# Kernel optimization log

Hardware: AMD Instinct MI355X
Metric: run time of the kernel (lower is better)

## Reference

```python
import jax, jax.numpy as jnp
import numpy as np

N_NODES = 50000
N_COLORS = 256
D = 64
H = 128  # MLP hidden = 2*D
E_VV = 800000
E_VC = 400000


def _mlp_params(key, d_in, d_hid, d_out):
    k1, k2 = jax.random.split(key)
    s1 = 1.0 / np.sqrt(d_in)
    s2 = 1.0 / np.sqrt(d_hid)
    return (
        jax.random.uniform(k1, (d_in, d_hid), jnp.float32, -s1, s1),
        jnp.zeros((d_hid,), jnp.float32),
        jax.random.uniform(k2, (d_hid, d_out), jnp.float32, -s2, s2),
        jnp.zeros((d_out,), jnp.float32),
    )


def setup_inputs() -> dict:
    key = jax.random.key(0)
    ks = jax.random.split(key, 8)
    x_v = jax.random.normal(ks[0], (N_NODES, D), jnp.float32)
    x_c = jax.random.normal(ks[1], (N_COLORS, D), jnp.float32)
    src_vv = jax.random.randint(ks[2], (E_VV,), 0, N_NODES, jnp.int32)
    dst_vv = jax.random.randint(ks[3], (E_VV,), 0, N_NODES, jnp.int32)
    src_vc = jax.random.randint(ks[4], (E_VC,), 0, N_COLORS, jnp.int32)
    dst_vc = jax.random.randint(ks[5], (E_VC,), 0, N_NODES, jnp.int32)
    W1v, b1v, W2v, b2v = _mlp_params(ks[6], D, H, D)
    W1c, b1c, W2c, b2c = _mlp_params(ks[7], D, H, D)
    return {
        "x_v": x_v, "x_c": x_c,
        "W1v": W1v, "b1v": b1v, "W2v": W2v, "b2v": b2v,
        "W1c": W1c, "b1c": b1c, "W2c": W2c, "b2c": b2c,
        "src_vv": src_vv, "dst_vv": dst_vv,
        "src_vc": src_vc, "dst_vc": dst_vc,
    }


def reference(x_v, x_c, W1v, b1v, W2v, b2v, W1c, b1c, W2c, b2c,
              src_vv, dst_vv, src_vc, dst_vc):
    n = x_v.shape[0]
    # vertex->vertex messages: gather, MLP, scatter-sum
    mv = jax.nn.relu(x_v[src_vv] @ W1v + b1v) @ W2v + b2v  # [E_vv, D]
    agg_v = jax.ops.segment_sum(mv, dst_vv, num_segments=n)
    # color->vertex messages: gather color embeddings, MLP, scatter-sum
    mc = jax.nn.relu(x_c[src_vc] @ W1c + b1c) @ W2c + b2c  # [E_vc, D]
    agg_c = jax.ops.segment_sum(mc, dst_vc, num_segments=n)
    return jax.nn.relu(x_v + agg_v + agg_c)
```

## Files before the change

### kernel.cpp

```cpp
#include <hip/hip_runtime.h>

#define NN 50000
#define NC 256
#define DD 64
#define HH 128
#define EVV 800000
#define EVC 400000
#define NE 1200000
#define NB 196
#define BCAP 8192
#define MLPV_B 3125
#define MLPC_B 16
#define MLP_B (MLPV_B + MLPC_B)
#define FILL_EPB 2048
#define FILL_B 586
#define K1_B (FILL_B * 7)
#define GAT_B (NB * 8)
#define VCAP 64

__device__ __forceinline__ unsigned short f2bf(float x) {
  unsigned u = __float_as_uint(x);
  u = (u + 0x7fffu + ((u >> 16) & 1u)) >> 16;
  return (unsigned short)u;
}

union SMem {
  struct {
    float xs[4][64][4];
    float hs[4][128][4];
  } m;
  struct {
    int cnt[NB];
    int off[NB];
    int gbase[NB];
    int sa[256], sb[256];
    unsigned int stage[FILL_EPB];
  } f;
};

__device__ __forceinline__ void mlp16(
    const float* __restrict__ X, const float* __restrict__ W1,
    const float* __restrict__ b1, const float* __restrict__ W2,
    const float* __restrict__ b2, unsigned short* __restrict__ Y, int blk,
    int nrows, float (*xs)[64][4], float (*hs)[128][4]) {
  const int wave = threadIdx.x >> 6;
  const int lane = threadIdx.x & 63;
  const int row0 = (blk * 4 + wave) * 4;

  {
    float4 a;
    a.x = (row0 + 0 < nrows) ? X[(row0 + 0) * DD + lane] : 0.f;
    a.y = (row0 + 1 < nrows) ? X[(row0 + 1) * DD + lane] : 0.f;
    a.z = (row0 + 2 < nrows) ? X[(row0 + 2) * DD + lane] : 0.f;
    a.w = (row0 + 3 < nrows) ? X[(row0 + 3) * DD + lane] : 0.f;
    *(float4*)&xs[wave][lane][0] = a;
  }

  const float bias0 = b1[lane];
  const float bias1 = b1[lane + 64];
  float h0[4], h1[4];
#pragma unroll
  for (int r = 0; r < 4; ++r) { h0[r] = bias0; h1[r] = bias1; }

#pragma unroll 8
  for (int k = 0; k < 64; ++k) {
    const float4 xa = *(const float4*)&xs[wave][k][0];
    const float wa = W1[k * HH + lane];
    const float wb = W1[k * HH + 64 + lane];
    h0[0] = fmaf(xa.x, wa, h0[0]); h1[0] = fmaf(xa.x, wb, h1[0]);
    h0[1] = fmaf(xa.y, wa, h0[1]); h1[1] = fmaf(xa.y, wb, h1[1]);
    h0[2] = fmaf(xa.z, wa, h0[2]); h1[2] = fmaf(xa.z, wb, h1[2]);
    h0[3] = fmaf(xa.w, wa, h0[3]); h1[3] = fmaf(xa.w, wb, h1[3]);
  }
  *(float4*)&hs[wave][lane][0] =
      make_float4(fmaxf(h0[0], 0.f), fmaxf(h0[1], 0.f), fmaxf(h0[2], 0.f),
                  fmaxf(h0[3], 0.f));
  *(float4*)&hs[wave][lane + 64][0] =
      make_float4(fmaxf(h1[0], 0.f), fmaxf(h1[1], 0.f), fmaxf(h1[2], 0.f),
                  fmaxf(h1[3], 0.f));

  const float bias2 = b2[lane];
  float a[4];
#pragma unroll
  for (int r = 0; r < 4; ++r) a[r] = bias2;

#pragma unroll 8
  for (int j = 0; j < HH; ++j) {
    const float4 ha = *(const float4*)&hs[wave][j][0];
    const float w = W2[j * DD + lane];
    a[0] = fmaf(ha.x, w, a[0]);
    a[1] = fmaf(ha.y, w, a[1]);
    a[2] = fmaf(ha.z, w, a[2]);
    a[3] = fmaf(ha.w, w, a[3]);
  }
#pragma unroll
  for (int r = 0; r < 4; ++r)
    if (row0 + r < nrows) Y[(row0 + r) * DD + lane] = f2bf(a[r]);
}

__device__ __forceinline__ void fill_block(
    const int* __restrict__ src_vv, const int* __restrict__ dst_vv,
    const int* __restrict__ src_vc, const int* __restrict__ dst_vc,
    int* __restrict__ gcur, unsigned int* __restrict__ records, int blk,
    SMem* sm) {
  const int t = threadIdx.x;
  const int base = blk * FILL_EPB;
  if (t < NB) sm->f.cnt[t] = 0;
  __syncthreads();

  unsigned int rec[8];
  int rk[8];
#pragma unroll
  for (int r = 0; r < 8; ++r) {
    const int e = base + r * 256 + t;
    rk[r] = -1;
    if (e < NE) {
      int s, d;
      if (e < EVV) {
        s = src_vv[e];
        d = dst_vv[e];
      } else {
        s = NN + src_vc[e - EVV];
        d = dst_vc[e - EVV];
      }
      rec[r] = ((unsigned int)d << 16) | (unsigned int)s;
      rk[r] = atomicAdd(&sm->f.cnt[d >> 8], 1);
    }
  }
  __syncthreads();

  const int val = (t < NB) ? sm->f.cnt[t] : 0;
  sm->f.sa[t] = val;
  __syncthreads();
  int* s = sm->f.sa;
  int* d = sm->f.sb;
  for (int o = 1; o < 256; o <<= 1) {
    d[t] = s[t] + ((t >= o) ? s[t - o] : 0);
    __syncthreads();
    int* tmp = s; s = d; d = tmp;
  }
  if (t < NB) {
    sm->f.off[t] = s[t] - val;
    sm->f.gbase[t] = t * BCAP + ((val > 0) ? atomicAdd(&gcur[t], val) : 0);
  }
  __syncthreads();

#pragma unroll
  for (int r = 0; r < 8; ++r)
    if (rk[r] >= 0) sm->f.stage[sm->f.off[rec[r] >> 24] + rk[r]] = rec[r];
  __syncthreads();

  const int total = (NE - base < FILL_EPB) ? (NE - base) : FILL_EPB;
  for (int i = t; i < total; i += 256) {
    const unsigned int u = sm->f.stage[i];
    const int b2 = u >> 24;
    records[sm->f.gbase[b2] + (i - sm->f.off[b2])] = u;
  }
}

__global__ __launch_bounds__(256) void k1_kernel(
    const float* __restrict__ x_v, const float* __restrict__ x_c,
    const float* __restrict__ W1v, const float* __restrict__ b1v,
    const float* __restrict__ W2v, const float* __restrict__ b2v,
    const float* __restrict__ W1c, const float* __restrict__ b1c,
    const float* __restrict__ W2c, const float* __restrict__ b2c,
    const int* __restrict__ src_vv, const int* __restrict__ dst_vv,
    const int* __restrict__ src_vc, const int* __restrict__ dst_vc,
    unsigned short* __restrict__ table, int* __restrict__ gcur,
    unsigned int* __restrict__ records) {
  __shared__ SMem sm;
  const int q = blockIdx.x / 7;
  const int r = blockIdx.x % 7;
  if (r == 0) {
    fill_block(src_vv, dst_vv, src_vc, dst_vc, gcur, records, q, &sm);
  } else {
    const int mb = q * 6 + (r - 1);
    if (mb >= MLP_B) return;
    if (mb < MLPV_B)
      mlp16(x_v, W1v, b1v, W2v, b2v, table, mb, NN, sm.m.xs, sm.m.hs);
    else
      mlp16(x_c, W1c, b1c, W2c, b2c, table + (size_t)NN * DD, mb - MLPV_B, NC,
            sm.m.xs, sm.m.hs);
  }
}

__device__ __forceinline__ void acc8(float* a, const uint4 t) {
  a[0] += __uint_as_float(t.x << 16);
  a[1] += __uint_as_float(t.x & 0xffff0000u);
  a[2] += __uint_as_float(t.y << 16);
  a[3] += __uint_as_float(t.y & 0xffff0000u);
  a[4] += __uint_as_float(t.z << 16);
  a[5] += __uint_as_float(t.z & 0xffff0000u);
  a[6] += __uint_as_float(t.w << 16);
  a[7] += __uint_as_float(t.w & 0xffff0000u);
}

__device__ __forceinline__ void place(unsigned int u, int sub, int* c1,
                                      unsigned short* slots) {
  const int dd = u >> 16;
  if (((dd >> 5) & 7) == sub) {
    const int lv = dd & 31;
    const int pos = atomicAdd(&c1[lv], 1);
    if (pos < VCAP) slots[lv * VCAP + pos] = (unsigned short)(u & 0xffffu);
  }
}

__global__ __launch_bounds__(256) void gather_kernel(
    const uint4* __restrict__ table4, const unsigned int* __restrict__ records,
    const int* __restrict__ gcur, const float4* __restrict__ xv4,
    float4* __restrict__ out4) {
  __shared__ int c1[32];
  __shared__ unsigned short slots[32 * VCAP];
  const int t = threadIdx.x;
  const int bucket = blockIdx.x >> 3;
  const int sub = blockIdx.x & 7;
  const int start = bucket * BCAP;
  const int nrec = gcur[bucket];

  const int g = t >> 3;
  const int c = t & 7;
  const int v = bucket * 256 + sub * 32 + g;
  const size_t ob = (size_t)v * 16 + c * 2;
  float4 x0 = {0.f, 0.f, 0.f, 0.f}, x1 = x0;
  if (v < NN) {
    x0 = xv4[ob];
    x1 = xv4[ob + 1];
  }

  if (t < 32) c1[t] = 0;
  __syncthreads();

  const uint4* rec4 = (const uint4*)(records + start);
  const int nfull = nrec >> 2;
  for (int q = t; q < nfull; q += 256) {
    const uint4 u = rec4[q];
    place(u.x, sub, c1, slots);
    place(u.y, sub, c1, slots);
    place(u.z, sub, c1, slots);
    place(u.w, sub, c1, slots);
  }
  for (int j = (nfull << 2) + t; j < nrec; j += 256)
    place(records[start + j], sub, c1, slots);
  __syncthreads();

  if (v >= NN) return;
  int n = c1[g];
  n = (n > VCAP) ? VCAP : n;
  const unsigned short* sl = slots + g * VCAP;

  float a[8];
#pragma unroll
  for (int r = 0; r < 8; ++r) a[r] = 0.f;

  int i = 0;
  for (; i + 8 <= n; i += 8) {
    const int e0 = sl[i + 0];
    const int e1 = sl[i + 1];
    const int e2 = sl[i + 2];
    const int e3 = sl[i + 3];
    const int e4 = sl[i + 4];
    const int e5 = sl[i + 5];
    const int e6 = sl[i + 6];
    const int e7 = sl[i + 7];
    const uint4 t0 = table4[(size_t)e0 * 8 + c];
    const uint4 t1 = table4[(size_t)e1 * 8 + c];
    const uint4 t2 = table4[(size_t)e2 * 8 + c];
    const uint4 t3 = table4[(size_t)e3 * 8 + c];
    const uint4 t4 = table4[(size_t)e4 * 8 + c];
    const uint4 t5 = table4[(size_t)e5 * 8 + c];
    const uint4 t6 = table4[(size_t)e6 * 8 + c];
    const uint4 t7 = table4[(size_t)e7 * 8 + c];
    acc8(a, t0); acc8(a, t1); acc8(a, t2); acc8(a, t3);
    acc8(a, t4); acc8(a, t5); acc8(a, t6); acc8(a, t7);
  }
  for (; i + 4 <= n; i += 4) {
    const int e0 = sl[i + 0];
    const int e1 = sl[i + 1];
    const int e2 = sl[i + 2];
    const int e3 = sl[i + 3];
    const uint4 t0 = table4[(size_t)e0 * 8 + c];
    const uint4 t1 = table4[(size_t)e1 * 8 + c];
    const uint4 t2 = table4[(size_t)e2 * 8 + c];
    const uint4 t3 = table4[(size_t)e3 * 8 + c];
    acc8(a, t0); acc8(a, t1); acc8(a, t2); acc8(a, t3);
  }
  for (; i < n; ++i) {
    const uint4 t0 = table4[(size_t)sl[i] * 8 + c];
    acc8(a, t0);
  }

  float4 o0, o1;
  o0.x = fmaxf(x0.x + a[0], 0.f);
  o0.y = fmaxf(x0.y + a[1], 0.f);
  o0.z = fmaxf(x0.z + a[2], 0.f);
  o0.w = fmaxf(x0.w + a[3], 0.f);
  o1.x = fmaxf(x1.x + a[4], 0.f);
  o1.y = fmaxf(x1.y + a[5], 0.f);
  o1.z = fmaxf(x1.z + a[6], 0.f);
  o1.w = fmaxf(x1.w + a[7], 0.f);
  out4[ob] = o0;
  out4[ob + 1] = o1;
}

extern "C" void kernel_launch(void* const* d_in, const int* in_sizes, int n_in,
                              void* d_out, int out_size, void* d_ws,
                              size_t ws_size, hipStream_t stream) {
  const float* x_v = (const float*)d_in[0];
  const float* x_c = (const float*)d_in[1];
  const float* W1v = (const float*)d_in[2];
  const float* b1v = (const float*)d_in[3];
  const float* W2v = (const float*)d_in[4];
  const float* b2v = (const float*)d_in[5];
  const float* W1c = (const float*)d_in[6];
  const float* b1c = (const float*)d_in[7];
  const float* W2c = (const float*)d_in[8];
  const float* b2c = (const float*)d_in[9];
  const int* src_vv = (const int*)d_in[10];
  const int* dst_vv = (const int*)d_in[11];
  const int* src_vc = (const int*)d_in[12];
  const int* dst_vc = (const int*)d_in[13];
  float* out = (float*)d_out;

  char* p = (char*)d_ws;
  unsigned short* table = (unsigned short*)p;
  p += (size_t)(NN + NC) * DD * sizeof(unsigned short);
  unsigned int* records = (unsigned int*)p;
  p += (size_t)NB * BCAP * sizeof(unsigned int);
  int* gcur = (int*)p;

  hipMemsetAsync(gcur, 0, NB * sizeof(int), stream);

  k1_kernel<<<K1_B, 256, 0, stream>>>(x_v, x_c, W1v, b1v, W2v, b2v, W1c, b1c,
                                      W2c, b2c, src_vv, dst_vv, src_vc, dst_vc,
                                      table, gcur, records);

  gather_kernel<<<GAT_B, 256, 0, stream>>>((const uint4*)table, records, gcur,
                                           (const float4*)x_v, (float4*)out);
}
```

Before: 150.8 us.

## Run node MLP on bf16 MFMA with pre-transposed weights and rebalanced block mix

Replaces the scalar FMA per-row MLP with 16x16x32 bf16 MFMA instructions, each wave handling 16 rows, with hidden activations staged in LDS as bf16. A new prep kernel transposes the weights and converts them to bf16 once per call. The fused launch grid is reshaped so each group of 7 blocks holds 3 fill blocks and 4 MLP blocks. This cuts the ALU cost of the MLP, at the cost of an extra launch and bf16 rounding of inputs and weights.

```diff
diff --git a/kernel.cpp b/kernel.cpp
--- a/kernel.cpp
+++ b/kernel.cpp
@@ -9,14 +9,19 @@
 #define NE 1200000
 #define NB 196
 #define BCAP 8192
-#define MLPV_B 3125
-#define MLPC_B 16
+#define MLPV_B 782
+#define MLPC_B 4
 #define MLP_B (MLPV_B + MLPC_B)
 #define FILL_EPB 2048
 #define FILL_B 586
-#define K1_B (FILL_B * 7)
+#define QUADS 197
+#define K1_B (QUADS * 7)
 #define GAT_B (NB * 8)
 #define VCAP 64
+#define HROW 136
+
+typedef __attribute__((ext_vector_type(8))) short bf16x8;
+typedef __attribute__((ext_vector_type(4))) float f32x4;
 
 __device__ __forceinline__ unsigned short f2bf(float x) {
   unsigned u = __float_as_uint(x);
@@ -25,10 +30,7 @@
 }
 
 union SMem {
-  struct {
-    float xs[4][64][4];
-    float hs[4][128][4];
-  } m;
+  unsigned short hl[4][16 * HROW];
   struct {
     int cnt[NB];
     int off[NB];
@@ -38,64 +40,95 @@
   } f;
 };
 
-__device__ __forceinline__ void mlp16(
-    const float* __restrict__ X, const float* __restrict__ W1,
-    const float* __restrict__ b1, const float* __restrict__ W2,
+__global__ __launch_bounds__(256) void prep_kernel(
+    const float* __restrict__ W1v, const float* __restrict__ W2v,
+    const float* __restrict__ W1c, const float* __restrict__ W2c,
+    unsigned short* __restrict__ wt) {
+  const int tid = blockIdx.x * 256 + threadIdx.x;
+  const int sel = tid >> 13;
+  const int t = tid & 8191;
+  unsigned short* dst = wt + sel * 8192;
+  if (sel == 0) {
+    const int n = t >> 6, k = t & 63;
+    dst[t] = f2bf(W1v[k * HH + n]);
+  } else if (sel == 1) {
+    const int n = t >> 7, k = t & 127;
+    dst[t] = f2bf(W2v[k * DD + n]);
+  } else if (sel == 2) {
+    const int n = t >> 6, k = t & 63;
+    dst[t] = f2bf(W1c[k * HH + n]);
+  } else {
+    const int n = t >> 7, k = t & 127;
+    dst[t] = f2bf(W2c[k * DD + n]);
+  }
+}
+
+__device__ __forceinline__ void mlp_mfma(
+    const float* __restrict__ X, const unsigned short* __restrict__ W1t,
+    const float* __restrict__ b1, const unsigned short* __restrict__ W2t,
     const float* __restrict__ b2, unsigned short* __restrict__ Y, int blk,
-    int nrows, float (*xs)[64][4], float (*hs)[128][4]) {
-  const int wave = threadIdx.x >> 6;
+    int nrows, unsigned short* __restrict__ hl) {
   const int lane = threadIdx.x & 63;
-  const int row0 = (blk * 4 + wave) * 4;
-
+  const int m = lane & 15;
+  const int quad = lane >> 4;
+  const int rowbase = blk * 64 + (threadIdx.x >> 6) * 16;
+
+  bf16x8 a0, a1;
   {
-    float4 a;
-    a.x = (row0 + 0 < nrows) ? X[(row0 + 0) * DD + lane] : 0.f;
-    a.y = (row0 + 1 < nrows) ? X[(row0 + 1) * DD + lane] : 0.f;
-    a.z = (row0 + 2 < nrows) ? X[(row0 + 2) * DD + lane] : 0.f;
-    a.w = (row0 + 3 < nrows) ? X[(row0 + 3) * DD + lane] : 0.f;
-    *(float4*)&xs[wave][lane][0] = a;
-  }
-
-  const float bias0 = b1[lane];
-  const float bias1 = b1[lane + 64];
-  float h0[4], h1[4];
-#pragma unroll
-  for (int r = 0; r < 4; ++r) { h0[r] = bias0; h1[r] = bias1; }
-
-#pragma unroll 8
-  for (int k = 0; k < 64; ++k) {
-    const float4 xa = *(const float4*)&xs[wave][k][0];
-    const float wa = W1[k * HH + lane];
-    const float wb = W1[k * HH + 64 + lane];
-    h0[0] = fmaf(xa.x, wa, h0[0]); h1[0] = fmaf(xa.x, wb, h1[0]);
-    h0[1] = fmaf(xa.y, wa, h0[1]); h1[1] = fmaf(xa.y, wb, h1[1]);
-    h0[2] = fmaf(xa.z, wa, h0[2]); h1[2] = fmaf(xa.z, wb, h1[2]);
-    h0[3] = fmaf(xa.w, wa, h0[3]); h1[3] = fmaf(xa.w, wb, h1[3]);
-  }
-  *(float4*)&hs[wave][lane][0] =
-      make_float4(fmaxf(h0[0], 0.f), fmaxf(h0[1], 0.f), fmaxf(h0[2], 0.f),
-                  fmaxf(h0[3], 0.f));
-  *(float4*)&hs[wave][lane + 64][0] =
-      make_float4(fmaxf(h1[0], 0.f), fmaxf(h1[1], 0.f), fmaxf(h1[2], 0.f),
-                  fmaxf(h1[3], 0.f));
-
-  const float bias2 = b2[lane];
-  float a[4];
-#pragma unroll
-  for (int r = 0; r < 4; ++r) a[r] = bias2;
-
-#pragma unroll 8
-  for (int j = 0; j < HH; ++j) {
-    const float4 ha = *(const float4*)&hs[wave][j][0];
-    const float w = W2[j * DD + lane];
-    a[0] = fmaf(ha.x, w, a[0]);
-    a[1] = fmaf(ha.y, w, a[1]);
-    a[2] = fmaf(ha.z, w, a[2]);
-    a[3] = fmaf(ha.w, w, a[3]);
-  }
-#pragma unroll
-  for (int r = 0; r < 4; ++r)
-    if (row0 + r < nrows) Y[(row0 + r) * DD + lane] = f2bf(a[r]);
+    float4 xa = {0.f, 0.f, 0.f, 0.f}, xb = xa, xc = xa, xd = xa;
+    const int row = rowbase + m;
+    if (row < nrows) {
+      const float* xp = X + (size_t)row * DD + quad * 8;
+      xa = *(const float4*)(xp);
+      xb = *(const float4*)(xp + 4);
+      xc = *(const float4*)(xp + 32);
+      xd = *(const float4*)(xp + 36);
+    }
+    a0[0] = (short)f2bf(xa.x); a0[1] = (short)f2bf(xa.y);
+    a0[2] = (short)f2bf(xa.z); a0[3] = (short)f2bf(xa.w);
+    a0[4] = (short)f2bf(xb.x); a0[5] = (short)f2bf(xb.y);
+    a0[6] = (short)f2bf(xb.z); a0[7] = (short)f2bf(xb.w);
+    a1[0] = (short)f2bf(xc.x); a1[1] = (short)f2bf(xc.y);
+    a1[2] = (short)f2bf(xc.z); a1[3] = (short)f2bf(xc.w);
+    a1[4] = (short)f2bf(xd.x); a1[5] = (short)f2bf(xd.y);
+    a1[6] = (short)f2bf(xd.z); a1[7] = (short)f2bf(xd.w);
+  }
+
+#pragma unroll
+  for (int nt = 0; nt < 8; ++nt) {
+    const int n = nt * 16 + m;
+    const float bv = b1[n];
+    f32x4 acc = {bv, bv, bv, bv};
+    const bf16x8 b0 = *(const bf16x8*)(W1t + n * 64 + quad * 8);
+    const bf16x8 b1f = *(const bf16x8*)(W1t + n * 64 + 32 + quad * 8);
+    acc = __builtin_amdgcn_mfma_f32_16x16x32_bf16(a0, b0, acc, 0, 0, 0);
+    acc = __builtin_amdgcn_mfma_f32_16x16x32_bf16(a1, b1f, acc, 0, 0, 0);
+#pragma unroll
+    for (int r = 0; r < 4; ++r)
+      hl[(quad * 4 + r) * HROW + n] = f2bf(fmaxf(acc[r], 0.f));
+  }
+
+  bf16x8 ha[4];
+#pragma unroll
+  for (int kc = 0; kc < 4; ++kc)
+    ha[kc] = *(const bf16x8*)(hl + m * HROW + kc * 32 + quad * 8);
+
+#pragma unroll
+  for (int nt = 0; nt < 4; ++nt) {
+    const int n = nt * 16 + m;
+    const float bv = b2[n];
+    f32x4 acc = {bv, bv, bv, bv};
+#pragma unroll
+    for (int kc = 0; kc < 4; ++kc) {
+      const bf16x8 bw = *(const bf16x8*)(W2t + n * 128 + kc * 32 + quad * 8);
+      acc = __builtin_amdgcn_mfma_f32_16x16x32_bf16(ha[kc], bw, acc, 0, 0, 0);
+    }
+#pragma unroll
+    for (int r = 0; r < 4; ++r) {
+      const int row = rowbase + quad * 4 + r;
+      if (row < nrows) Y[(size_t)row * DD + n] = f2bf(acc[r]);
+    }
+  }
 }
 
 __device__ __forceinline__ void fill_block(
@@ -160,10 +193,9 @@
 
 __global__ __launch_bounds__(256) void k1_kernel(
     const float* __restrict__ x_v, const float* __restrict__ x_c,
-    const float* __restrict__ W1v, const float* __restrict__ b1v,
-    const float* __restrict__ W2v, const float* __restrict__ b2v,
-    const float* __restrict__ W1c, const float* __restrict__ b1c,
-    const float* __restrict__ W2c, const float* __restrict__ b2c,
+    const float* __restrict__ b1v, const float* __restrict__ b2v,
+    const float* __restrict__ b1c, const float* __restrict__ b2c,
+    const unsigned short* __restrict__ wt,
     const int* __restrict__ src_vv, const int* __restrict__ dst_vv,
     const int* __restrict__ src_vc, const int* __restrict__ dst_vc,
     unsigned short* __restrict__ table, int* __restrict__ gcur,
@@ -171,16 +203,19 @@
   __shared__ SMem sm;
   const int q = blockIdx.x / 7;
   const int r = blockIdx.x % 7;
-  if (r == 0) {
-    fill_block(src_vv, dst_vv, src_vc, dst_vc, gcur, records, q, &sm);
+  if (r < 3) {
+    const int fid = q * 3 + r;
+    if (fid >= FILL_B) return;
+    fill_block(src_vv, dst_vv, src_vc, dst_vc, gcur, records, fid, &sm);
   } else {
-    const int mb = q * 6 + (r - 1);
+    const int mb = q * 4 + (r - 3);
     if (mb >= MLP_B) return;
+    unsigned short* hl = sm.hl[threadIdx.x >> 6];
     if (mb < MLPV_B)
-      mlp16(x_v, W1v, b1v, W2v, b2v, table, mb, NN, sm.m.xs, sm.m.hs);
+      mlp_mfma(x_v, wt, b1v, wt + 8192, b2v, table, mb, NN, hl);
     else
-      mlp16(x_c, W1c, b1c, W2c, b2c, table + (size_t)NN * DD, mb - MLPV_B, NC,
-            sm.m.xs, sm.m.hs);
+      mlp_mfma(x_c, wt + 16384, b1c, wt + 24576, b2c,
+               table + (size_t)NN * DD, mb - MLPV_B, NC, hl);
   }
 }
 
@@ -326,13 +361,17 @@
   p += (size_t)(NN + NC) * DD * sizeof(unsigned short);
   unsigned int* records = (unsigned int*)p;
   p += (size_t)NB * BCAP * sizeof(unsigned int);
+  unsigned short* wt = (unsigned short*)p;
+  p += (size_t)4 * 8192 * sizeof(unsigned short);
   int* gcur = (int*)p;
 
   hipMemsetAsync(gcur, 0, NB * sizeof(int), stream);
 
-  k1_kernel<<<K1_B, 256, 0, stream>>>(x_v, x_c, W1v, b1v, W2v, b2v, W1c, b1c,
-                                      W2c, b2c, src_vv, dst_vv, src_vc, dst_vc,
-                                      table, gcur, records);
+  prep_kernel<<<128, 256, 0, stream>>>(W1v, W2v, W1c, W2c, wt);
+
+  k1_kernel<<<K1_B, 256, 0, stream>>>(x_v, x_c, b1v, b2v, b1c, b2c, wt,
+                                      src_vv, dst_vv, src_vc, dst_vc, table,
+                                      gcur, records);
 
   gather_kernel<<<GAT_B, 256, 0, stream>>>((const uint4*)table, records, gcur,
                                            (const float4*)x_v, (float4*)out);
```

Result: faster. 144.2 us (-4.4%).
